# Kernel optimization log

Measured on AMD Instinct MI355X. Metric: run time of the kernel, lower is better.

## Reference

```python
import jax, jax.numpy as jnp
import numpy as np

B, N, D, H, E = 32, 512, 512, 8, 4
HD = D // H
EPS = 1e-3  # keras LayerNormalization default epsilon
NEG = -1e9  # keras Softmax masking additive constant


def _ln(x, g, b):
    m = jnp.mean(x, axis=-1, keepdims=True)
    v = jnp.mean(jnp.square(x - m), axis=-1, keepdims=True)
    return (x - m) * jax.lax.rsqrt(v + EPS) * g + b


def setup_inputs() -> dict:
    key = jax.random.key(0)
    ks = jax.random.split(key, 16)
    s = 0.02
    return {
        "x": jax.random.normal(ks[0], (B, N, D), jnp.float32),
        "mask": jax.random.randint(ks[1], (B, 1, N, N), 0, 2) > 0,
        "interaction": jax.random.normal(ks[2], (B, N, N, H), jnp.float32),
        "w_qkv": jax.random.normal(ks[3], (D, 3 * D), jnp.float32) * s,
        "b_qkv": jnp.zeros((3 * D,), jnp.float32),
        "w_out": jax.random.normal(ks[4], (D, D), jnp.float32) * s,
        "b_out": jnp.zeros((D,), jnp.float32),
        "w1": jax.random.normal(ks[5], (D, E * D), jnp.float32) * s,
        "b1": jnp.zeros((E * D,), jnp.float32),
        "w2": jax.random.normal(ks[6], (E * D, D), jnp.float32) * s,
        "b2": jnp.zeros((D,), jnp.float32),
        "g_pre": jnp.ones((D,), jnp.float32), "be_pre": jnp.zeros((D,), jnp.float32),
        "g_post": jnp.ones((D,), jnp.float32), "be_post": jnp.zeros((D,), jnp.float32),
        "g_ffn": jnp.ones((D,), jnp.float32), "be_ffn": jnp.zeros((D,), jnp.float32),
        "g_mid": jnp.ones((E * D,), jnp.float32), "be_mid": jnp.zeros((E * D,), jnp.float32),
    }


def reference(x, mask, interaction, w_qkv, b_qkv, w_out, b_out, w1, b1, w2, b2,
              g_pre, be_pre, g_post, be_post, g_ffn, be_ffn, g_mid, be_mid):
    # pre-LN MHSA
    h = _ln(x, g_pre, be_pre)
    qkv = h @ w_qkv + b_qkv                           # [B,N,3D]
    qkv = qkv.reshape(B, N, 3, H, HD)
    q, k, v = (jnp.transpose(qkv[:, :, i], (0, 2, 1, 3)) for i in range(3))  # [B,H,N,HD]
    scores = jnp.einsum('bhnd,bhmd->bhnm', q, k) / np.sqrt(HD).astype(np.float32)
    scores = scores + jnp.transpose(interaction, (0, 3, 1, 2))  # per-head additive bias
    scores = scores + (1.0 - mask.astype(scores.dtype)) * NEG   # keras Softmax mask semantics
    attn = jax.nn.softmax(scores, axis=-1)
    o = jnp.einsum('bhnm,bhmd->bhnd', attn, v)
    o = jnp.transpose(o, (0, 2, 1, 3)).reshape(B, N, D)
    o = o @ w_out + b_out
    attended = _ln(o, g_post, be_post) + x            # post-MHSA LN then residual
    # FFN with mid-LN
    f = _ln(attended, g_ffn, be_ffn)
    f = jax.nn.gelu(f @ w1 + b1, approximate=False)
    f = _ln(f, g_mid, be_mid)
    f = f @ w2 + b2
    return f + attended
```

## Files before the change

### kernel.cpp

```cpp
#include <hip/hip_runtime.h>
#include <hip/hip_bf16.h>
#include <math.h>

constexpr int CB = 32, CN = 512, CD = 512, CH = 8, CHD = 64;
constexpr float LN_EPS = 1e-3f;

typedef _Float16 half8 __attribute__((ext_vector_type(8)));
typedef _Float16 half4v __attribute__((ext_vector_type(4)));
typedef float f32x4 __attribute__((ext_vector_type(4)));

__device__ __forceinline__ void async16(const void* g, void* l) {
    __builtin_amdgcn_global_load_lds((const __attribute__((address_space(1))) void*)g,
                                     (__attribute__((address_space(3))) void*)l, 16, 0, 0);
}

__global__ __launch_bounds__(256) void transpose_f16(const float* __restrict__ in,
                                                     _Float16* __restrict__ out,
                                                     int K, int N) {
    __shared__ float t[32][33];
    const int tx = threadIdx.x % 32, ty = threadIdx.x / 32;
    const int n0 = blockIdx.x * 32, k0 = blockIdx.y * 32;
#pragma unroll
    for (int i = 0; i < 4; ++i)
        t[ty + i * 8][tx] = in[(size_t)(k0 + ty + i * 8) * N + n0 + tx];
    __syncthreads();
#pragma unroll
    for (int i = 0; i < 4; ++i)
        out[(size_t)(n0 + ty + i * 8) * K + k0 + tx] = (_Float16)t[tx][ty + i * 8];
}

__global__ __launch_bounds__(256) void bias_prepass(const float* __restrict__ inter,
        const int* __restrict__ mask, _Float16* __restrict__ bias, int b0) {
    const size_t idx = (size_t)blockIdx.x * 256 + threadIdx.x;
    const size_t gidx = (size_t)b0 * CN * CN + idx;
    float4 v0 = *(const float4*)(inter + gidx * 8);
    float4 v1 = *(const float4*)(inter + gidx * 8 + 4);
    const float add = mask[gidx] ? 0.f : -30000.f;
    const float vals[8] = {v0.x, v0.y, v0.z, v0.w, v1.x, v1.y, v1.z, v1.w};
    const size_t plane = (size_t)CN * CN;
    const size_t bl = idx / plane;
    const size_t nm = idx % plane;
    _Float16* outp = bias + bl * CH * plane + nm;
#pragma unroll
    for (int h = 0; h < 8; ++h) outp[h * plane] = (_Float16)(vals[h] + add);
}

template<int WIDTH, bool IN_F16, bool OUT_F16, bool ADDRES>
__global__ __launch_bounds__(256) void ln2_kernel(const void* __restrict__ in_,
        const float* __restrict__ g, const float* __restrict__ be,
        const float* __restrict__ res, void* __restrict__ out_) {
    constexpr int NPL = WIDTH / 64;
    const int row = blockIdx.x * 4 + (threadIdx.x >> 6);
    const int lane = threadIdx.x & 63;
    const int c0 = lane * NPL;
    float v[NPL];
    if (IN_F16) {
        const _Float16* p = (const _Float16*)in_ + (size_t)row * WIDTH + c0;
#pragma unroll
        for (int i = 0; i < NPL / 8; ++i) {
            half8 u = *(const half8*)(p + i * 8);
#pragma unroll
            for (int j = 0; j < 8; ++j) v[i * 8 + j] = (float)u[j];
        }
    } else {
        const float* p = (const float*)in_ + (size_t)row * WIDTH + c0;
#pragma unroll
        for (int i = 0; i < NPL / 4; ++i) {
            float4 u = *(const float4*)(p + i * 4);
            v[i * 4 + 0] = u.x; v[i * 4 + 1] = u.y; v[i * 4 + 2] = u.z; v[i * 4 + 3] = u.w;
        }
    }
    float s1 = 0.f, s2 = 0.f;
#pragma unroll
    for (int i = 0; i < NPL; ++i) { s1 += v[i]; s2 += v[i] * v[i]; }
#pragma unroll
    for (int off = 1; off < 64; off <<= 1) { s1 += __shfl_xor(s1, off); s2 += __shfl_xor(s2, off); }
    const float mean = s1 * (1.0f / WIDTH);
    const float var = s2 * (1.0f / WIDTH) - mean * mean;
    const float rstd = rsqrtf(var + LN_EPS);

    float ov[NPL];
#pragma unroll
    for (int i = 0; i < NPL / 4; ++i) {
        float4 gv = *(const float4*)(g + c0 + i * 4);
        float4 bv = *(const float4*)(be + c0 + i * 4);
        ov[i * 4 + 0] = (v[i * 4 + 0] - mean) * rstd * gv.x + bv.x;
        ov[i * 4 + 1] = (v[i * 4 + 1] - mean) * rstd * gv.y + bv.y;
        ov[i * 4 + 2] = (v[i * 4 + 2] - mean) * rstd * gv.z + bv.z;
        ov[i * 4 + 3] = (v[i * 4 + 3] - mean) * rstd * gv.w + bv.w;
    }
    if (ADDRES) {
        const float* rp = res + (size_t)row * WIDTH + c0;
#pragma unroll
        for (int i = 0; i < NPL / 4; ++i) {
            float4 rv = *(const float4*)(rp + i * 4);
            ov[i * 4 + 0] += rv.x; ov[i * 4 + 1] += rv.y; ov[i * 4 + 2] += rv.z; ov[i * 4 + 3] += rv.w;
        }
    }
    if (OUT_F16) {
        _Float16* po = (_Float16*)out_ + (size_t)row * WIDTH + c0;
#pragma unroll
        for (int i = 0; i < NPL / 8; ++i) {
            half8 hv;
#pragma unroll
            for (int j = 0; j < 8; ++j) hv[j] = (_Float16)ov[i * 8 + j];
            *(half8*)(po + i * 8) = hv;
        }
    } else {
        float* po = (float*)out_ + (size_t)row * WIDTH + c0;
#pragma unroll
        for (int i = 0; i < NPL / 4; ++i) {
            float4 w = make_float4(ov[i * 4 + 0], ov[i * 4 + 1], ov[i * 4 + 2], ov[i * 4 + 3]);
            *(float4*)(po + i * 4) = w;
        }
    }
}

template<bool GELU, bool RES, bool OUT_F16>
__global__ __launch_bounds__(256) void gemm_f16(const _Float16* __restrict__ A,
        const _Float16* __restrict__ Wt, const float* __restrict__ bias,
        const float* __restrict__ res, void* __restrict__ Cout,
        int M, int N, int K) {
    __shared__ __align__(16) char As[16384];
    __shared__ __align__(16) char Bs[16384];
    const int tid = threadIdx.x;
    const int nbx = N >> 7;
    const int nwg = (M >> 7) * nbx;
    int gb = blockIdx.x;
    gb = (gb & 7) * (nwg >> 3) + (gb >> 3);
    const int by = gb / nbx, bx = gb % nbx;

    const int lane = tid & 63;
    const int wv = tid >> 6;
    const int rsub = lane >> 3;
    const int slot = lane & 7;
    const int chunk = slot ^ rsub;
    const _Float16* Abase = A + (size_t)(by * 128) * K + chunk * 8;
    const _Float16* Bbase = Wt + (size_t)(bx * 128) * K + chunk * 8;

    const int wm = wv >> 1, wn = wv & 1;
    const int lrow = lane & 15;
    const int lk = lane >> 4;
    const int xorv = lane & 7;
    const int aRowB = (wm * 64 + lrow) * 128;
    const int bRowB = (wn * 64 + lrow) * 128;

    f32x4 acc[4][4] = {};

    for (int k0 = 0; k0 < K; k0 += 64) {
#pragma unroll
        for (int t = 0; t < 4; ++t) {
            const int rowb = t * 32 + wv * 8;
            async16(Abase + (size_t)(rowb + rsub) * K + k0, As + rowb * 128);
            async16(Bbase + (size_t)(rowb + rsub) * K + k0, Bs + rowb * 128);
        }
        __syncthreads();
#pragma unroll
        for (int kk = 0; kk < 2; ++kk) {
            const int sa = ((kk * 4 + lk) ^ xorv) << 4;
            half8 af[4], bf[4];
#pragma unroll
            for (int mi = 0; mi < 4; ++mi) af[mi] = *(const half8*)(As + aRowB + mi * 2048 + sa);
#pragma unroll
            for (int ni = 0; ni < 4; ++ni) bf[ni] = *(const half8*)(Bs + bRowB + ni * 2048 + sa);
#pragma unroll
            for (int mi = 0; mi < 4; ++mi)
#pragma unroll
                for (int ni = 0; ni < 4; ++ni)
                    acc[mi][ni] = __builtin_amdgcn_mfma_f32_16x16x32_f16(af[mi], bf[ni], acc[mi][ni], 0, 0, 0);
        }
        __syncthreads();
    }

    const int lr4 = (lane >> 4) * 4;
    const int lc = lane & 15;
#pragma unroll
    for (int ni = 0; ni < 4; ++ni) {
        const int colg = bx * 128 + wn * 64 + ni * 16 + lc;
        const float bv = bias[colg];
#pragma unroll
        for (int mi = 0; mi < 4; ++mi) {
            const int rowg = by * 128 + wm * 64 + mi * 16 + lr4;
#pragma unroll
            for (int r = 0; r < 4; ++r) {
                float v = acc[mi][ni][r] + bv;
                if (GELU) v = 0.5f * v * (1.0f + erff(v * 0.70710678118654752440f));
                if (RES) v += res[(size_t)(rowg + r) * N + colg];
                if (OUT_F16) ((_Float16*)Cout)[(size_t)(rowg + r) * N + colg] = (_Float16)v;
                else ((float*)Cout)[(size_t)(rowg + r) * N + colg] = v;
            }
        }
    }
}

__global__ __launch_bounds__(256) void attn_mfma(
        const _Float16* __restrict__ qkv, const _Float16* __restrict__ bias,
        _Float16* __restrict__ o, int b0) {
    const int bid = blockIdx.x;
    const int h  = bid & 7;
    const int qt = (bid >> 3) & 7;
    const int bl = bid >> 6;
    const int b  = b0 + bl;
    const int tid = threadIdx.x;
    const int lane = tid & 63;
    const int w = tid >> 6;
    const int l15 = lane & 15, l4 = lane >> 4;

    __shared__ __align__(16) char Qs[8192];
    __shared__ __align__(16) char Ks[8192];
    __shared__ __align__(16) char Vt[8192];
    __shared__ __align__(16) char Ps[8192];

    constexpr size_t QKVROW = 1536;
    {
        const _Float16* Qg = qkv + (size_t)(b * CN + qt * 64) * QKVROW + h * 64;
#pragma unroll
        for (int p = 0; p < 2; ++p) {
            const int f = tid + 256 * p;
            const int r = f >> 3, c = f & 7;
            half8 v = *(const half8*)(Qg + (size_t)r * QKVROW + c * 8);
            *(half8*)(Qs + r * 128 + ((c ^ (r & 7)) << 4)) = v;
        }
    }

    f32x4 acc_o[4] = {};
    float m_run[4] = {-3e38f, -3e38f, -3e38f, -3e38f};
    float l_run[4] = {0.f, 0.f, 0.f, 0.f};

    const _Float16* biasBase = bias + ((size_t)(bl * CH + h) * CN + qt * 64) * CN;

    for (int mt = 0; mt < 8; ++mt) {
        __syncthreads();
        const _Float16* Kg = qkv + (size_t)(b * CN + mt * 64) * QKVROW + 512 + h * 64;
        const _Float16* Vg = Kg + 512;
#pragma unroll
        for (int p = 0; p < 2; ++p) {
            const int f = tid + 256 * p;
            const int r = f >> 3, c = f & 7;
            half8 kv = *(const half8*)(Kg + (size_t)r * QKVROW + c * 8);
            *(half8*)(Ks + r * 128 + ((c ^ (r & 7)) << 4)) = kv;
        }
#pragma unroll
        for (int p = 0; p < 2; ++p) {
            const int f = tid + 256 * p;
            const int m = f >> 3, dc = f & 7;
            half8 vv = *(const half8*)(Vg + (size_t)m * QKVROW + dc * 8);
            const int mc = m >> 3, mo = m & 7;
#pragma unroll
            for (int j = 0; j < 8; ++j) {
                const int d = dc * 8 + j;
                *(_Float16*)(Vt + d * 128 + ((mc ^ (d & 7)) << 4) + mo * 2) = vv[j];
            }
        }
        __syncthreads();

        f32x4 acc_s[4] = {};
#pragma unroll
        for (int step = 0; step < 2; ++step) {
            const int qrow = w * 16 + l15;
            const int ch = step * 4 + l4;
            half8 aq = *(const half8*)(Qs + qrow * 128 + ((ch ^ (qrow & 7)) << 4));
#pragma unroll
            for (int mi = 0; mi < 4; ++mi) {
                const int mrow = mi * 16 + l15;
                half8 bk = *(const half8*)(Ks + mrow * 128 + ((ch ^ (mrow & 7)) << 4));
                acc_s[mi] = __builtin_amdgcn_mfma_f32_16x16x32_f16(aq, bk, acc_s[mi], 0, 0, 0);
            }
        }
#pragma unroll
        for (int r = 0; r < 4; ++r) {
            const _Float16* brow = biasBase + (size_t)(w * 16 + l4 * 4 + r) * CN + mt * 64 + l15;
            float pv[4];
            float rmax = -3e38f;
#pragma unroll
            for (int mi = 0; mi < 4; ++mi) {
                float s = acc_s[mi][r] * 0.125f + (float)brow[mi * 16];
                pv[mi] = s;
                rmax = fmaxf(rmax, s);
            }
#pragma unroll
            for (int off = 1; off < 16; off <<= 1) rmax = fmaxf(rmax, __shfl_xor(rmax, off));
            const float nm = fmaxf(m_run[r], rmax);
            const float fac = __expf(m_run[r] - nm);
            m_run[r] = nm;
            float ps = 0.f;
#pragma unroll
            for (int mi = 0; mi < 4; ++mi) { float e = __expf(pv[mi] - nm); pv[mi] = e; ps += e; }
#pragma unroll
            for (int off = 1; off < 16; off <<= 1) ps += __shfl_xor(ps, off);
            l_run[r] = l_run[r] * fac + ps;
#pragma unroll
            for (int di = 0; di < 4; ++di) acc_o[di][r] *= fac;
            const int qrow = w * 16 + l4 * 4 + r;
#pragma unroll
            for (int mi = 0; mi < 4; ++mi) {
                const int m = mi * 16 + l15;
                *(_Float16*)(Ps + qrow * 128 + (((m >> 3) ^ (qrow & 7)) << 4) + (m & 7) * 2) = (_Float16)pv[mi];
            }
        }
#pragma unroll
        for (int step = 0; step < 2; ++step) {
            const int qrow = w * 16 + l15;
            const int ch = step * 4 + l4;
            half8 ap = *(const half8*)(Ps + qrow * 128 + ((ch ^ (qrow & 7)) << 4));
#pragma unroll
            for (int di = 0; di < 4; ++di) {
                const int drow = di * 16 + l15;
                half8 bv = *(const half8*)(Vt + drow * 128 + ((ch ^ (drow & 7)) << 4));
                acc_o[di] = __builtin_amdgcn_mfma_f32_16x16x32_f16(ap, bv, acc_o[di], 0, 0, 0);
            }
        }
    }
    _Float16* orow = o + (size_t)(b * CN + qt * 64 + w * 16 + l4 * 4) * CD + h * 64 + l15;
#pragma unroll
    for (int r = 0; r < 4; ++r) {
        const float inv = 1.0f / l_run[r];
#pragma unroll
        for (int di = 0; di < 4; ++di)
            orow[(size_t)r * CD + di * 16] = (_Float16)(acc_o[di][r] * inv);
    }
}

extern "C" void kernel_launch(void* const* d_in, const int* in_sizes, int n_in,
                              void* d_out, int out_size, void* d_ws, size_t ws_size,
                              hipStream_t stream) {
    const float* x      = (const float*)d_in[0];
    const int*   mask   = (const int*)d_in[1];
    const float* inter  = (const float*)d_in[2];
    const float* w_qkv  = (const float*)d_in[3];
    const float* b_qkv  = (const float*)d_in[4];
    const float* w_out  = (const float*)d_in[5];
    const float* b_out  = (const float*)d_in[6];
    const float* w1     = (const float*)d_in[7];
    const float* b1     = (const float*)d_in[8];
    const float* w2     = (const float*)d_in[9];
    const float* b2     = (const float*)d_in[10];
    const float* g_pre  = (const float*)d_in[11];
    const float* be_pre = (const float*)d_in[12];
    const float* g_post = (const float*)d_in[13];
    const float* be_post= (const float*)d_in[14];
    const float* g_ffn  = (const float*)d_in[15];
    const float* be_ffn = (const float*)d_in[16];
    const float* g_mid  = (const float*)d_in[17];
    const float* be_mid = (const float*)d_in[18];
    float* out = (float*)d_out;

    char* ws = (char*)d_ws;
    const size_t MB = 1ull << 20;
    _Float16* wt_qkv = (_Float16*)(ws + 0 * MB);
    _Float16* wt_out = (_Float16*)(ws + 2 * MB);
    _Float16* wt_w1  = (_Float16*)(ws + 3 * MB);
    _Float16* wt_w2  = (_Float16*)(ws + 5 * MB);
    float*    attended = (float*)(ws + 8 * MB);
    _Float16* biasb  = (_Float16*)(ws + 40 * MB);
    void*     bigbuf = (void*)(ws + 40 * MB);
    _Float16* qkvb   = (_Float16*)(ws + 104 * MB);
    _Float16* hb     = (_Float16*)(ws + 152 * MB);
    _Float16* ob     = (_Float16*)(ws + 168 * MB);

    const int M = CB * CN;

    transpose_f16<<<dim3(1536 / 32, 512 / 32), 256, 0, stream>>>(w_qkv, wt_qkv, 512, 1536);
    transpose_f16<<<dim3(512 / 32, 512 / 32), 256, 0, stream>>>(w_out, wt_out, 512, 512);
    transpose_f16<<<dim3(2048 / 32, 512 / 32), 256, 0, stream>>>(w1, wt_w1, 512, 2048);
    transpose_f16<<<dim3(512 / 32, 2048 / 32), 256, 0, stream>>>(w2, wt_w2, 2048, 512);

    ln2_kernel<512, false, true, false><<<M / 4, 256, 0, stream>>>(x, g_pre, be_pre, nullptr, hb);
    gemm_f16<false, false, true><<<(M / 128) * (1536 / 128), 256, 0, stream>>>(
        hb, wt_qkv, b_qkv, nullptr, qkvb, M, 1536, 512);
    for (int half = 0; half < 2; ++half) {
        const int b0 = half * 16;
        bias_prepass<<<16 * CN * CN / 256, 256, 0, stream>>>(inter, mask, biasb, b0);
        attn_mfma<<<16 * 8 * 8, 256, 0, stream>>>(qkvb, biasb, ob, b0);
    }
    gemm_f16<false, false, false><<<(M / 128) * (512 / 128), 256, 0, stream>>>(
        ob, wt_out, b_out, nullptr, bigbuf, M, 512, 512);
    ln2_kernel<512, false, false, true><<<M / 4, 256, 0, stream>>>(bigbuf, g_post, be_post, x, attended);
    ln2_kernel<512, false, true, false><<<M / 4, 256, 0, stream>>>(attended, g_ffn, be_ffn, nullptr, hb);
    gemm_f16<true, false, true><<<(M / 128) * (2048 / 128), 256, 0, stream>>>(
        hb, wt_w1, b1, nullptr, bigbuf, M, 2048, 512);
    ln2_kernel<2048, true, true, false><<<M / 4, 256, 0, stream>>>(bigbuf, g_mid, be_mid, nullptr, bigbuf);
    gemm_f16<false, true, false><<<(M / 128) * (512 / 128), 256, 0, stream>>>(
        (_Float16*)bigbuf, wt_w2, b2, attended, out, M, 512, 2048);
}
```

Baseline: 484.8 us.

## Fuse bias/mask into attention, merge post and FFN layernorms, XCD-aware block mapping

Removes the bias_prepass kernel and reads the interaction tensor and mask directly inside the attention kernel, adding them to the scores in registers. Attention now launches once over all batches, with a block-index remap that places each batch's blocks on the same XCD. The out-projection writes f16, and the post-MHSA LN, residual add and FFN LN are fused into one kernel. The interaction reads are strided by H (8 floats apart per head), which could make the attention loads uncoalesced in exchange for skipping the f16 bias round trip.

```diff
diff --git a/kernel.cpp b/kernel.cpp
--- a/kernel.cpp
+++ b/kernel.cpp
@@ -6,7 +6,6 @@
 constexpr float LN_EPS = 1e-3f;
 
 typedef _Float16 half8 __attribute__((ext_vector_type(8)));
-typedef _Float16 half4v __attribute__((ext_vector_type(4)));
 typedef float f32x4 __attribute__((ext_vector_type(4)));
 
 __device__ __forceinline__ void async16(const void* g, void* l) {
@@ -27,22 +26,6 @@
 #pragma unroll
     for (int i = 0; i < 4; ++i)
         out[(size_t)(n0 + ty + i * 8) * K + k0 + tx] = (_Float16)t[tx][ty + i * 8];
-}
-
-__global__ __launch_bounds__(256) void bias_prepass(const float* __restrict__ inter,
-        const int* __restrict__ mask, _Float16* __restrict__ bias, int b0) {
-    const size_t idx = (size_t)blockIdx.x * 256 + threadIdx.x;
-    const size_t gidx = (size_t)b0 * CN * CN + idx;
-    float4 v0 = *(const float4*)(inter + gidx * 8);
-    float4 v1 = *(const float4*)(inter + gidx * 8 + 4);
-    const float add = mask[gidx] ? 0.f : -30000.f;
-    const float vals[8] = {v0.x, v0.y, v0.z, v0.w, v1.x, v1.y, v1.z, v1.w};
-    const size_t plane = (size_t)CN * CN;
-    const size_t bl = idx / plane;
-    const size_t nm = idx % plane;
-    _Float16* outp = bias + bl * CH * plane + nm;
-#pragma unroll
-    for (int h = 0; h < 8; ++h) outp[h * plane] = (_Float16)(vals[h] + add);
 }
 
 template<int WIDTH, bool IN_F16, bool OUT_F16, bool ADDRES>
@@ -114,6 +97,56 @@
             *(float4*)(po + i * 4) = w;
         }
     }
+}
+
+__global__ __launch_bounds__(256) void ln_post_ffn(const _Float16* __restrict__ o2,
+        const float* __restrict__ x,
+        const float* __restrict__ g_post, const float* __restrict__ be_post,
+        const float* __restrict__ g_ffn, const float* __restrict__ be_ffn,
+        float* __restrict__ attended, _Float16* __restrict__ f) {
+    constexpr int NPL = 8;
+    const int row = blockIdx.x * 4 + (threadIdx.x >> 6);
+    const int lane = threadIdx.x & 63;
+    const int c0 = lane * NPL;
+    float v[NPL], xv[NPL];
+    {
+        half8 u = *(const half8*)(o2 + (size_t)row * CD + c0);
+#pragma unroll
+        for (int j = 0; j < 8; ++j) v[j] = (float)u[j];
+        float4 a = *(const float4*)(x + (size_t)row * CD + c0);
+        float4 b = *(const float4*)(x + (size_t)row * CD + c0 + 4);
+        xv[0] = a.x; xv[1] = a.y; xv[2] = a.z; xv[3] = a.w;
+        xv[4] = b.x; xv[5] = b.y; xv[6] = b.z; xv[7] = b.w;
+    }
+    float s1 = 0.f, s2 = 0.f;
+#pragma unroll
+    for (int i = 0; i < NPL; ++i) { s1 += v[i]; s2 += v[i] * v[i]; }
+#pragma unroll
+    for (int off = 1; off < 64; off <<= 1) { s1 += __shfl_xor(s1, off); s2 += __shfl_xor(s2, off); }
+    float mean = s1 * (1.0f / CD);
+    float rstd = rsqrtf(s2 * (1.0f / CD) - mean * mean + LN_EPS);
+    float av[NPL];
+#pragma unroll
+    for (int i = 0; i < NPL; ++i)
+        av[i] = (v[i] - mean) * rstd * g_post[c0 + i] + be_post[c0 + i] + xv[i];
+    {
+        float4 w0 = make_float4(av[0], av[1], av[2], av[3]);
+        float4 w1 = make_float4(av[4], av[5], av[6], av[7]);
+        *(float4*)(attended + (size_t)row * CD + c0) = w0;
+        *(float4*)(attended + (size_t)row * CD + c0 + 4) = w1;
+    }
+    s1 = 0.f; s2 = 0.f;
+#pragma unroll
+    for (int i = 0; i < NPL; ++i) { s1 += av[i]; s2 += av[i] * av[i]; }
+#pragma unroll
+    for (int off = 1; off < 64; off <<= 1) { s1 += __shfl_xor(s1, off); s2 += __shfl_xor(s2, off); }
+    mean = s1 * (1.0f / CD);
+    rstd = rsqrtf(s2 * (1.0f / CD) - mean * mean + LN_EPS);
+    half8 hv;
+#pragma unroll
+    for (int i = 0; i < NPL; ++i)
+        hv[i] = (_Float16)((av[i] - mean) * rstd * g_ffn[c0 + i] + be_ffn[c0 + i]);
+    *(half8*)(f + (size_t)row * CD + c0) = hv;
 }
 
 template<bool GELU, bool RES, bool OUT_F16>
@@ -194,13 +227,14 @@
 }
 
 __global__ __launch_bounds__(256) void attn_mfma(
-        const _Float16* __restrict__ qkv, const _Float16* __restrict__ bias,
-        _Float16* __restrict__ o, int b0) {
+        const _Float16* __restrict__ qkv, const float* __restrict__ inter,
+        const int* __restrict__ mask, _Float16* __restrict__ o) {
     const int bid = blockIdx.x;
-    const int h  = bid & 7;
-    const int qt = (bid >> 3) & 7;
-    const int bl = bid >> 6;
-    const int b  = b0 + bl;
+    const int xcd = bid & 7;
+    const int s = bid >> 3;
+    const int h = s & 7;
+    const int qt = (s >> 3) & 7;
+    const int b = (s >> 6) * 8 + xcd;
     const int tid = threadIdx.x;
     const int lane = tid & 63;
     const int w = tid >> 6;
@@ -227,7 +261,14 @@
     float m_run[4] = {-3e38f, -3e38f, -3e38f, -3e38f};
     float l_run[4] = {0.f, 0.f, 0.f, 0.f};
 
-    const _Float16* biasBase = bias + ((size_t)(bl * CH + h) * CN + qt * 64) * CN;
+    const int qg0 = qt * 64 + w * 16 + l4 * 4;
+    const float* interB[4];
+    const int* maskB[4];
+#pragma unroll
+    for (int r = 0; r < 4; ++r) {
+        interB[r] = inter + ((size_t)(b * CN + qg0 + r) * CN) * CH + h;
+        maskB[r]  = mask + (size_t)(b * CN + qg0 + r) * CN;
+    }
 
     for (int mt = 0; mt < 8; ++mt) {
         __syncthreads();
@@ -252,6 +293,15 @@
                 *(_Float16*)(Vt + d * 128 + ((mc ^ (d & 7)) << 4) + mo * 2) = vv[j];
             }
         }
+        float iv[4][4];
+#pragma unroll
+        for (int r = 0; r < 4; ++r)
+#pragma unroll
+            for (int mi = 0; mi < 4; ++mi) {
+                const int m = mt * 64 + mi * 16 + l15;
+                const float bvv = interB[r][(size_t)m * CH];
+                iv[r][mi] = bvv + (maskB[r][m] ? 0.f : -1e9f);
+            }
         __syncthreads();
 
         f32x4 acc_s[4] = {};
@@ -269,14 +319,13 @@
         }
 #pragma unroll
         for (int r = 0; r < 4; ++r) {
-            const _Float16* brow = biasBase + (size_t)(w * 16 + l4 * 4 + r) * CN + mt * 64 + l15;
             float pv[4];
             float rmax = -3e38f;
 #pragma unroll
             for (int mi = 0; mi < 4; ++mi) {
-                float s = acc_s[mi][r] * 0.125f + (float)brow[mi * 16];
-                pv[mi] = s;
-                rmax = fmaxf(rmax, s);
+                float sv = acc_s[mi][r] * 0.125f + iv[r][mi];
+                pv[mi] = sv;
+                rmax = fmaxf(rmax, sv);
             }
 #pragma unroll
             for (int off = 1; off < 16; off <<= 1) rmax = fmaxf(rmax, __shfl_xor(rmax, off));
@@ -352,11 +401,12 @@
     _Float16* wt_w1  = (_Float16*)(ws + 3 * MB);
     _Float16* wt_w2  = (_Float16*)(ws + 5 * MB);
     float*    attended = (float*)(ws + 8 * MB);
-    _Float16* biasb  = (_Float16*)(ws + 40 * MB);
-    void*     bigbuf = (void*)(ws + 40 * MB);
-    _Float16* qkvb   = (_Float16*)(ws + 104 * MB);
-    _Float16* hb     = (_Float16*)(ws + 152 * MB);
-    _Float16* ob     = (_Float16*)(ws + 168 * MB);
+    _Float16* o2h    = (_Float16*)(ws + 40 * MB);
+    _Float16* f1b    = (_Float16*)(ws + 64 * MB);
+    _Float16* qkvb   = (_Float16*)(ws + 128 * MB);
+    _Float16* hb     = (_Float16*)(ws + 176 * MB);
+    _Float16* ob     = (_Float16*)(ws + 192 * MB);
+    _Float16* fb     = (_Float16*)(ws + 208 * MB);
 
     const int M = CB * CN;
 
@@ -368,18 +418,13 @@
     ln2_kernel<512, false, true, false><<<M / 4, 256, 0, stream>>>(x, g_pre, be_pre, nullptr, hb);
     gemm_f16<false, false, true><<<(M / 128) * (1536 / 128), 256, 0, stream>>>(
         hb, wt_qkv, b_qkv, nullptr, qkvb, M, 1536, 512);
-    for (int half = 0; half < 2; ++half) {
-        const int b0 = half * 16;
-        bias_prepass<<<16 * CN * CN / 256, 256, 0, stream>>>(inter, mask, biasb, b0);
-        attn_mfma<<<16 * 8 * 8, 256, 0, stream>>>(qkvb, biasb, ob, b0);
-    }
-    gemm_f16<false, false, false><<<(M / 128) * (512 / 128), 256, 0, stream>>>(
-        ob, wt_out, b_out, nullptr, bigbuf, M, 512, 512);
-    ln2_kernel<512, false, false, true><<<M / 4, 256, 0, stream>>>(bigbuf, g_post, be_post, x, attended);
-    ln2_kernel<512, false, true, false><<<M / 4, 256, 0, stream>>>(attended, g_ffn, be_ffn, nullptr, hb);
+    attn_mfma<<<CB * 8 * 8, 256, 0, stream>>>(qkvb, inter, mask, ob);
+    gemm_f16<false, false, true><<<(M / 128) * (512 / 128), 256, 0, stream>>>(
+        ob, wt_out, b_out, nullptr, o2h, M, 512, 512);
+    ln_post_ffn<<<M / 4, 256, 0, stream>>>(o2h, x, g_post, be_post, g_ffn, be_ffn, attended, fb);
     gemm_f16<true, false, true><<<(M / 128) * (2048 / 128), 256, 0, stream>>>(
-        hb, wt_w1, b1, nullptr, bigbuf, M, 2048, 512);
-    ln2_kernel<2048, true, true, false><<<M / 4, 256, 0, stream>>>(bigbuf, g_mid, be_mid, nullptr, bigbuf);
+        fb, wt_w1, b1, nullptr, f1b, M, 2048, 512);
+    ln2_kernel<2048, true, true, false><<<M / 4, 256, 0, stream>>>(f1b, g_mid, be_mid, nullptr, f1b);
     gemm_f16<false, true, false><<<(M / 128) * (512 / 128), 256, 0, stream>>>(
-        (_Float16*)bigbuf, wt_w2, b2, attended, out, M, 512, 2048);
-}
+        f1b, wt_w2, b2, attended, out, M, 512, 2048);
+}
```

Result: faster. 460.9 us (-4.9%).
